# Performance work log

Hardware: AMD Instinct MI355X
Metric: run time of the kernel (lower is better)

Reference implementation:

```python
import jax, jax.numpy as jnp
import numpy as np

EPS = 1e-15  # matches torch_geometric dense pooling EPS


def gcn_conv(x, src, dst, w, W, b, n):
    # GCNConv(normalize=False): linear first, then weighted scatter-add src->dst, then bias
    h = x @ W
    msg = w[:, None] * h[src]  # [E, out]
    return jax.ops.segment_sum(msg, dst, num_segments=n) + b


def setup_inputs() -> dict:
    key = jax.random.key(0)
    ks = jax.random.split(key, 8)
    N, E, d, k = 12288, 393216, 256, 16
    x = jax.random.normal(ks[0], (N, d), dtype=jnp.float32)
    edge_index = jax.random.randint(ks[1], (2, E), 0, N, dtype=jnp.int32)
    edge_weight = jax.random.uniform(ks[2], (E,), dtype=jnp.float32)
    sc = 1.0 / np.sqrt(d).astype(np.float32)
    W1 = jax.random.normal(ks[3], (d, d), dtype=jnp.float32) * sc
    b1 = jnp.zeros((d,), jnp.float32)
    W2 = jax.random.normal(ks[4], (d, d), dtype=jnp.float32) * sc
    b2 = jnp.zeros((d,), jnp.float32)
    Wm = jax.random.normal(ks[5], (d, k), dtype=jnp.float32) * sc
    bm = jnp.zeros((k,), jnp.float32)
    return dict(x=x, edge_weight=edge_weight, W1=W1, b1=b1, W2=W2, b2=b2,
                Wm=Wm, bm=bm, edge_index=edge_index)


def reference(x, edge_weight, W1, b1, W2, b2, Wm, bm, edge_index):
    src, dst = edge_index[0], edge_index[1]
    n = x.shape[0]
    # message-passing stack: GCNConv -> ReLU -> GCNConv -> ReLU
    h = jax.nn.relu(gcn_conv(x, src, dst, edge_weight, W1, b1, n))
    h = jax.nn.relu(gcn_conv(h, src, dst, edge_weight, W2, b2, n))
    # cluster MLP (single Linear, Identity activations)
    s_logits = h @ Wm + bm  # [N, k]
    # to_dense_adj(edge_index, edge_attr=edge_weight): dense [N, N]
    adj = jnp.zeros((n, n), x.dtype).at[src, dst].add(edge_weight)
    # just_balance_pool (batch of 1)
    s = jax.nn.softmax(s_logits, axis=-1)  # [N, k]
    out = s.T @ h              # pooled features (unused by module output)
    out_adj = s.T @ adj @ s    # pooled adjacency (unused by module output)
    gram = s.T @ s             # [k, k]
    k = s.shape[-1]
    b_loss = -jnp.trace(jnp.sqrt(gram + EPS)) / jnp.sqrt(jnp.float32(n * k))
    return s, b_loss
```

## Files before the change

### kernel.cpp

```cpp
#include <hip/hip_runtime.h>
#include <hip/hip_bf16.h>
#include <hip/hip_fp16.h>

#define D 256
#define KCL 16
#define EPS 1e-15f
#define PAD 128

typedef __attribute__((ext_vector_type(8))) short short8;
typedef __attribute__((ext_vector_type(8))) _Float16 half8;
typedef __attribute__((ext_vector_type(4))) float f32x4;

__global__ __launch_bounds__(256) void setup_k(const float* __restrict__ W1,
                                               const float* __restrict__ W2,
                                               __half* __restrict__ Wt1,
                                               __half* __restrict__ Wt2,
                                               const int* __restrict__ src,
                                               const int* __restrict__ dst,
                                               const float* __restrict__ ew,
                                               int* __restrict__ deg,
                                               int2* __restrict__ edges, int E) {
    int b = blockIdx.x;
    if (b < 512) {
        const float* W = (b < 256) ? W1 : W2;
        __half* T = (b < 256) ? Wt1 : Wt2;
        int c = b & 255;
        int k = threadIdx.x;
        T[(size_t)c * D + k] = __float2half(W[(size_t)k * D + c]);
    } else {
        int e = (b - 512) * 256 + threadIdx.x;
        if (e < E) {
            int d = dst[e];
            int slot = atomicAdd(&deg[d], 1);
            if (slot < PAD)
                edges[(size_t)d * PAD + slot] = make_int2(src[e], __float_as_int(ew[e]));
        }
    }
}

__device__ __forceinline__ short8 ld8h(const float* p) {
    float4 v0 = *(const float4*)p;
    float4 v1 = *(const float4*)(p + 4);
    float vv[8] = {v0.x, v0.y, v0.z, v0.w, v1.x, v1.y, v1.z, v1.w};
    short8 o;
#pragma unroll
    for (int j = 0; j < 8; ++j) {
        _Float16 h = (_Float16)vv[j];
        o[j] = __builtin_bit_cast(short, h);
    }
    return o;
}
__device__ __forceinline__ short8 ld8h(const __half* p) {
    return *(const short8*)p;
}

template<typename T>
__global__ __launch_bounds__(256) void gemm_k(const T* __restrict__ A,
                                              const __half* __restrict__ Bt,
                                              __half* __restrict__ C) {
    __shared__ short Ah[64][40];
    int tid = threadIdx.x;
    int lane = tid & 63, w = tid >> 6;
    int bm = blockIdx.x * 64, bn = blockIdx.y * 64;
    f32x4 acc[4];
#pragma unroll
    for (int i = 0; i < 4; ++i) acc[i] = (f32x4){0.f, 0.f, 0.f, 0.f};

    int r  = tid >> 2;
    int cc = (tid & 3) * 8;
    int ar = w * 16 + (lane & 15);
    int kq = (lane >> 4) * 8;

    for (int kk = 0; kk < D; kk += 32) {
        short8 a8 = ld8h(&A[(size_t)(bm + r) * D + kk + cc]);
        __syncthreads();
        *(short8*)&Ah[r][cc] = a8;
        __syncthreads();

        half8 av = __builtin_bit_cast(half8, *(const short8*)&Ah[ar][kq]);
#pragma unroll
        for (int nf = 0; nf < 4; ++nf) {
            int col = bn + nf * 16 + (lane & 15);
            half8 bv = __builtin_bit_cast(half8,
                        *(const short8*)&Bt[(size_t)col * D + kk + kq]);
            acc[nf] = __builtin_amdgcn_mfma_f32_16x16x32_f16(av, bv, acc[nf], 0, 0, 0);
        }
    }
    int rbase = bm + w * 16 + (lane >> 4) * 4;
    int cb = bn + (lane & 15);
#pragma unroll
    for (int nf = 0; nf < 4; ++nf)
#pragma unroll
        for (int rr = 0; rr < 4; ++rr)
            C[(size_t)(rbase + rr) * D + cb + nf * 16] = __float2half(acc[nf][rr]);
}

__device__ __forceinline__ void spmm_wave(const __half* __restrict__ h,
                                          const int2* __restrict__ edges,
                                          int node, int n, int lane,
                                          int2* se, float f[4]) {
    if (lane < n) se[lane] = edges[(size_t)node * PAD + lane];
    if (lane + 64 < n) se[lane + 64] = edges[(size_t)node * PAD + lane + 64];
    float a0 = 0.f, a1 = 0.f, a2 = 0.f, a3 = 0.f;
    int i = 0;
    for (; i + 4 <= n; i += 4) {
        int2 e0 = se[i], e1 = se[i + 1], e2 = se[i + 2], e3 = se[i + 3];
        float2 r0 = ((const float2*)(h + (size_t)e0.x * D))[lane];
        float2 r1 = ((const float2*)(h + (size_t)e1.x * D))[lane];
        float2 r2 = ((const float2*)(h + (size_t)e2.x * D))[lane];
        float2 r3 = ((const float2*)(h + (size_t)e3.x * D))[lane];
        float w0 = __int_as_float(e0.y), w1 = __int_as_float(e1.y);
        float w2 = __int_as_float(e2.y), w3 = __int_as_float(e3.y);
        float2 p, q;
        p = __half22float2(__builtin_bit_cast(__half2, r0.x));
        q = __half22float2(__builtin_bit_cast(__half2, r0.y));
        a0 = fmaf(w0, p.x, a0); a1 = fmaf(w0, p.y, a1);
        a2 = fmaf(w0, q.x, a2); a3 = fmaf(w0, q.y, a3);
        p = __half22float2(__builtin_bit_cast(__half2, r1.x));
        q = __half22float2(__builtin_bit_cast(__half2, r1.y));
        a0 = fmaf(w1, p.x, a0); a1 = fmaf(w1, p.y, a1);
        a2 = fmaf(w1, q.x, a2); a3 = fmaf(w1, q.y, a3);
        p = __half22float2(__builtin_bit_cast(__half2, r2.x));
        q = __half22float2(__builtin_bit_cast(__half2, r2.y));
        a0 = fmaf(w2, p.x, a0); a1 = fmaf(w2, p.y, a1);
        a2 = fmaf(w2, q.x, a2); a3 = fmaf(w2, q.y, a3);
        p = __half22float2(__builtin_bit_cast(__half2, r3.x));
        q = __half22float2(__builtin_bit_cast(__half2, r3.y));
        a0 = fmaf(w3, p.x, a0); a1 = fmaf(w3, p.y, a1);
        a2 = fmaf(w3, q.x, a2); a3 = fmaf(w3, q.y, a3);
    }
    for (; i < n; ++i) {
        int2 e = se[i];
        float2 r = ((const float2*)(h + (size_t)e.x * D))[lane];
        float wv = __int_as_float(e.y);
        float2 p = __half22float2(__builtin_bit_cast(__half2, r.x));
        float2 q = __half22float2(__builtin_bit_cast(__half2, r.y));
        a0 = fmaf(wv, p.x, a0); a1 = fmaf(wv, p.y, a1);
        a2 = fmaf(wv, q.x, a2); a3 = fmaf(wv, q.y, a3);
    }
    f[0] = a0; f[1] = a1; f[2] = a2; f[3] = a3;
}

__global__ __launch_bounds__(256) void spmm_k(const __half* __restrict__ h,
                                              const int2* __restrict__ edges,
                                              const int* __restrict__ deg,
                                              const float* __restrict__ bias,
                                              __half* __restrict__ out) {
    __shared__ int2 se[4][PAD];
    int tid = threadIdx.x;
    int wv = tid >> 6, lane = tid & 63;
    int node = blockIdx.x * 4 + wv;
    int n = min(deg[node], PAD);
    float f[4];
    spmm_wave(h, edges, node, n, lane, se[wv], f);
    float4 bv = ((const float4*)bias)[lane];
    __half2 o01 = __float22half2_rn(make_float2(fmaxf(f[0] + bv.x, 0.f),
                                                fmaxf(f[1] + bv.y, 0.f)));
    __half2 o23 = __float22half2_rn(make_float2(fmaxf(f[2] + bv.z, 0.f),
                                                fmaxf(f[3] + bv.w, 0.f)));
    ((float2*)(out + (size_t)node * D))[lane] =
        make_float2(__builtin_bit_cast(float, o01), __builtin_bit_cast(float, o23));
}

__global__ __launch_bounds__(256) void spmm_cluster_k(const __half* __restrict__ h,
                                                      const int2* __restrict__ edges,
                                                      const int* __restrict__ deg,
                                                      const float* __restrict__ bias,
                                                      const float* __restrict__ Wm,
                                                      const float* __restrict__ bmv,
                                                      float* __restrict__ s_out) {
    __shared__ int2 se[4][PAD];
    int tid = threadIdx.x;
    int wv = tid >> 6, lane = tid & 63;
    int node = blockIdx.x * 4 + wv;
    int n = min(deg[node], PAD);
    float f[4];
    spmm_wave(h, edges, node, n, lane, se[wv], f);
    float4 bv = ((const float4*)bias)[lane];
    f[0] = fmaxf(f[0] + bv.x, 0.f); f[1] = fmaxf(f[1] + bv.y, 0.f);
    f[2] = fmaxf(f[2] + bv.z, 0.f); f[3] = fmaxf(f[3] + bv.w, 0.f);

    float pl[KCL];
#pragma unroll
    for (int j = 0; j < KCL; ++j) pl[j] = 0.f;
#pragma unroll
    for (int u = 0; u < 4; ++u) {
        const float4* wr = (const float4*)&Wm[(size_t)(4 * lane + u) * KCL];
        float fv = f[u];
#pragma unroll
        for (int q = 0; q < 4; ++q) {
            float4 a = wr[q];
            pl[q * 4 + 0] = fmaf(fv, a.x, pl[q * 4 + 0]);
            pl[q * 4 + 1] = fmaf(fv, a.y, pl[q * 4 + 1]);
            pl[q * 4 + 2] = fmaf(fv, a.z, pl[q * 4 + 2]);
            pl[q * 4 + 3] = fmaf(fv, a.w, pl[q * 4 + 3]);
        }
    }
#pragma unroll
    for (int off = 32; off; off >>= 1)
#pragma unroll
        for (int j = 0; j < KCL; ++j) pl[j] += __shfl_xor(pl[j], off, 64);
    if (lane == 0) {
        float mx = -1e30f;
#pragma unroll
        for (int j = 0; j < KCL; ++j) { pl[j] += bmv[j]; mx = fmaxf(mx, pl[j]); }
        float sum = 0.f;
#pragma unroll
        for (int j = 0; j < KCL; ++j) { pl[j] = __expf(pl[j] - mx); sum += pl[j]; }
        float inv = 1.f / sum;
        float* so = &s_out[(size_t)node * KCL];
#pragma unroll
        for (int q = 0; q < 4; ++q)
            *(float4*)&so[q * 4] = make_float4(pl[q*4+0] * inv, pl[q*4+1] * inv,
                                               pl[q*4+2] * inv, pl[q*4+3] * inv);
    }
}

__global__ __launch_bounds__(256) void sqloss_k(const float* __restrict__ s,
                                                float* __restrict__ diag,
                                                int* __restrict__ done,
                                                float* __restrict__ loss_out, int N) {
    int tid = threadIdx.x;
    int j = tid & 15;
    int g = tid >> 4;
    int total = N * KCL;
    float acc = 0.f;
    for (int idx = blockIdx.x * 256 + tid; idx < total; idx += gridDim.x * 256) {
        float v = s[idx];
        acc = fmaf(v, v, acc);
    }
    __shared__ float red[16][17];
    red[g][j] = acc;
    __syncthreads();
    if (g == 0) {
        float a = red[0][j];
#pragma unroll
        for (int gg = 1; gg < 16; ++gg) a += red[gg][j];
        atomicAdd(&diag[j], a);
    }
    __threadfence();
    __shared__ int lastFlag;
    if (tid == 0) {
        int old = atomicAdd(done, 1);
        lastFlag = (old == (int)gridDim.x - 1);
    }
    __syncthreads();
    if (lastFlag && tid == 0) {
        __threadfence();
        float sum = 0.f;
#pragma unroll
        for (int jj = 0; jj < KCL; ++jj) {
            float v = atomicAdd(&diag[jj], 0.f);
            sum += sqrtf(v + EPS);
        }
        loss_out[0] = -sum / sqrtf((float)N * (float)KCL);
    }
}

extern "C" void kernel_launch(void* const* d_in, const int* in_sizes, int n_in,
                              void* d_out, int out_size, void* d_ws, size_t ws_size,
                              hipStream_t stream) {
    const float* x  = (const float*)d_in[0];
    const float* ew = (const float*)d_in[1];
    const float* W1 = (const float*)d_in[2];
    const float* b1 = (const float*)d_in[3];
    const float* W2 = (const float*)d_in[4];
    const float* b2 = (const float*)d_in[5];
    const float* Wm = (const float*)d_in[6];
    const float* bm = (const float*)d_in[7];
    const int*   ei = (const int*)d_in[8];

    const int N = in_sizes[0] / D;
    const int E = in_sizes[1];
    const int* src = ei;
    const int* dst = ei + E;

    float* out = (float*)d_out;

    char* ws = (char*)d_ws;
    __half* G    = (__half*)ws;       ws += (size_t)N * D * 2;
    __half* H1   = (__half*)ws;       ws += (size_t)N * D * 2;
    int*   deg   = (int*)ws;          ws += (size_t)N * 4;
    float* diag  = (float*)ws;        ws += 64;
    int*   done  = (int*)ws;          ws += 16;
    int2*  edges = (int2*)ws;         ws += (size_t)N * PAD * 8;
    __half* Wt1  = (__half*)ws;       ws += (size_t)D * D * 2;
    __half* Wt2  = (__half*)ws;       ws += (size_t)D * D * 2;

    hipMemsetAsync(deg, 0, (size_t)N * 4 + 80, stream);
    int gE = (E + 255) / 256;
    setup_k<<<512 + gE, 256, 0, stream>>>(W1, W2, Wt1, Wt2,
                                          src, dst, ew, deg, edges, E);

    dim3 ggrid(N / 64, 4);
    gemm_k<float><<<ggrid, 256, 0, stream>>>(x, Wt1, G);
    spmm_k<<<N / 4, 256, 0, stream>>>(G, edges, deg, b1, H1);
    gemm_k<__half><<<ggrid, 256, 0, stream>>>(H1, Wt2, G);
    spmm_cluster_k<<<N / 4, 256, 0, stream>>>(G, edges, deg, b2, Wm, bm, out);
    sqloss_k<<<64, 256, 0, stream>>>(out, diag, done, out + (size_t)N * KCL, N);
}
```

Measured before the change: 214.0 us.

## Split SpMM feature dimension across two blocks and fuse softmax with loss

Each SpMM node is now handled by two blocks, each covering half of the 256 features, so twice as many waves are in flight for the gather-bound aggregation. Block ids are interleaved so that both halves of a node run near each other in time. The cluster projection writes per-half partial logits, and a new kernel sums them, applies softmax, and accumulates the squared-sum loss in a single pass. Edge lists are loaded with nontemporal hints. In exchange, edge lists are read twice, gather requests become 4-byte instead of 8-byte, and a partial-logit buffer is written and then read back.

```diff
diff --git a/kernel.cpp b/kernel.cpp
--- a/kernel.cpp
+++ b/kernel.cpp
@@ -6,10 +6,16 @@
 #define KCL 16
 #define EPS 1e-15f
 #define PAD 128
+#define HPF 128
 
 typedef __attribute__((ext_vector_type(8))) short short8;
 typedef __attribute__((ext_vector_type(8))) _Float16 half8;
 typedef __attribute__((ext_vector_type(4))) float f32x4;
+
+__device__ __forceinline__ int2 ntload_i2(const int2* p) {
+    long long v = __builtin_nontemporal_load((const long long*)p);
+    return *(int2*)&v;
+}
 
 __global__ __launch_bounds__(256) void setup_k(const float* __restrict__ W1,
                                                const float* __restrict__ W2,
@@ -95,149 +101,159 @@
             C[(size_t)(rbase + rr) * D + cb + nf * 16] = __float2half(acc[nf][rr]);
 }
 
-__device__ __forceinline__ void spmm_wave(const __half* __restrict__ h,
-                                          const int2* __restrict__ edges,
-                                          int node, int n, int lane,
-                                          int2* se, float f[4]) {
-    if (lane < n) se[lane] = edges[(size_t)node * PAD + lane];
-    if (lane + 64 < n) se[lane + 64] = edges[(size_t)node * PAD + lane + 64];
-    float a0 = 0.f, a1 = 0.f, a2 = 0.f, a3 = 0.f;
+__device__ __forceinline__ void spmm_wave_half(const __half* __restrict__ h,
+                                               const int2* __restrict__ edges,
+                                               int node, int half, int n, int lane,
+                                               int2* se, float& o0, float& o1) {
+    if (lane < n) se[lane] = ntload_i2(&edges[(size_t)node * PAD + lane]);
+    if (lane + 64 < n) se[lane + 64] = ntload_i2(&edges[(size_t)node * PAD + lane + 64]);
+    float a0 = 0.f, a1 = 0.f;
     int i = 0;
     for (; i + 4 <= n; i += 4) {
         int2 e0 = se[i], e1 = se[i + 1], e2 = se[i + 2], e3 = se[i + 3];
-        float2 r0 = ((const float2*)(h + (size_t)e0.x * D))[lane];
-        float2 r1 = ((const float2*)(h + (size_t)e1.x * D))[lane];
-        float2 r2 = ((const float2*)(h + (size_t)e2.x * D))[lane];
-        float2 r3 = ((const float2*)(h + (size_t)e3.x * D))[lane];
+        float r0 = ((const float*)(h + (size_t)e0.x * D + half * HPF))[lane];
+        float r1 = ((const float*)(h + (size_t)e1.x * D + half * HPF))[lane];
+        float r2 = ((const float*)(h + (size_t)e2.x * D + half * HPF))[lane];
+        float r3 = ((const float*)(h + (size_t)e3.x * D + half * HPF))[lane];
         float w0 = __int_as_float(e0.y), w1 = __int_as_float(e1.y);
         float w2 = __int_as_float(e2.y), w3 = __int_as_float(e3.y);
-        float2 p, q;
-        p = __half22float2(__builtin_bit_cast(__half2, r0.x));
-        q = __half22float2(__builtin_bit_cast(__half2, r0.y));
+        float2 p;
+        p = __half22float2(__builtin_bit_cast(__half2, r0));
         a0 = fmaf(w0, p.x, a0); a1 = fmaf(w0, p.y, a1);
-        a2 = fmaf(w0, q.x, a2); a3 = fmaf(w0, q.y, a3);
-        p = __half22float2(__builtin_bit_cast(__half2, r1.x));
-        q = __half22float2(__builtin_bit_cast(__half2, r1.y));
+        p = __half22float2(__builtin_bit_cast(__half2, r1));
         a0 = fmaf(w1, p.x, a0); a1 = fmaf(w1, p.y, a1);
-        a2 = fmaf(w1, q.x, a2); a3 = fmaf(w1, q.y, a3);
-        p = __half22float2(__builtin_bit_cast(__half2, r2.x));
-        q = __half22float2(__builtin_bit_cast(__half2, r2.y));
+        p = __half22float2(__builtin_bit_cast(__half2, r2));
         a0 = fmaf(w2, p.x, a0); a1 = fmaf(w2, p.y, a1);
-        a2 = fmaf(w2, q.x, a2); a3 = fmaf(w2, q.y, a3);
-        p = __half22float2(__builtin_bit_cast(__half2, r3.x));
-        q = __half22float2(__builtin_bit_cast(__half2, r3.y));
+        p = __half22float2(__builtin_bit_cast(__half2, r3));
         a0 = fmaf(w3, p.x, a0); a1 = fmaf(w3, p.y, a1);
-        a2 = fmaf(w3, q.x, a2); a3 = fmaf(w3, q.y, a3);
     }
     for (; i < n; ++i) {
         int2 e = se[i];
-        float2 r = ((const float2*)(h + (size_t)e.x * D))[lane];
+        float r = ((const float*)(h + (size_t)e.x * D + half * HPF))[lane];
         float wv = __int_as_float(e.y);
-        float2 p = __half22float2(__builtin_bit_cast(__half2, r.x));
-        float2 q = __half22float2(__builtin_bit_cast(__half2, r.y));
+        float2 p = __half22float2(__builtin_bit_cast(__half2, r));
         a0 = fmaf(wv, p.x, a0); a1 = fmaf(wv, p.y, a1);
-        a2 = fmaf(wv, q.x, a2); a3 = fmaf(wv, q.y, a3);
-    }
-    f[0] = a0; f[1] = a1; f[2] = a2; f[3] = a3;
-}
-
-__global__ __launch_bounds__(256) void spmm_k(const __half* __restrict__ h,
-                                              const int2* __restrict__ edges,
-                                              const int* __restrict__ deg,
-                                              const float* __restrict__ bias,
-                                              __half* __restrict__ out) {
+    }
+    o0 = a0; o1 = a1;
+}
+
+__device__ __forceinline__ void decode_bid(int bid, int& half, int& quad) {
+    half = (bid & 7) >> 2;
+    quad = ((bid >> 3) << 2) | (bid & 3);
+}
+
+__global__ __launch_bounds__(256) void spmm1_k(const __half* __restrict__ h,
+                                               const int2* __restrict__ edges,
+                                               const int* __restrict__ deg,
+                                               const float* __restrict__ bias,
+                                               __half* __restrict__ out) {
     __shared__ int2 se[4][PAD];
+    int half, quad;
+    decode_bid(blockIdx.x, half, quad);
     int tid = threadIdx.x;
     int wv = tid >> 6, lane = tid & 63;
-    int node = blockIdx.x * 4 + wv;
+    int node = quad * 4 + wv;
     int n = min(deg[node], PAD);
-    float f[4];
-    spmm_wave(h, edges, node, n, lane, se[wv], f);
-    float4 bv = ((const float4*)bias)[lane];
-    __half2 o01 = __float22half2_rn(make_float2(fmaxf(f[0] + bv.x, 0.f),
-                                                fmaxf(f[1] + bv.y, 0.f)));
-    __half2 o23 = __float22half2_rn(make_float2(fmaxf(f[2] + bv.z, 0.f),
-                                                fmaxf(f[3] + bv.w, 0.f)));
-    ((float2*)(out + (size_t)node * D))[lane] =
-        make_float2(__builtin_bit_cast(float, o01), __builtin_bit_cast(float, o23));
-}
-
-__global__ __launch_bounds__(256) void spmm_cluster_k(const __half* __restrict__ h,
-                                                      const int2* __restrict__ edges,
-                                                      const int* __restrict__ deg,
-                                                      const float* __restrict__ bias,
-                                                      const float* __restrict__ Wm,
-                                                      const float* __restrict__ bmv,
-                                                      float* __restrict__ s_out) {
+    float f0, f1;
+    spmm_wave_half(h, edges, node, half, n, lane, se[wv], f0, f1);
+    float2 bv = ((const float2*)(bias + half * HPF))[lane];
+    __half2 o = __float22half2_rn(make_float2(fmaxf(f0 + bv.x, 0.f),
+                                              fmaxf(f1 + bv.y, 0.f)));
+    __builtin_nontemporal_store(__builtin_bit_cast(unsigned, o),
+        (unsigned*)&((__half2*)(out + (size_t)node * D + half * HPF))[lane]);
+}
+
+__global__ __launch_bounds__(256) void spmm2_k(const __half* __restrict__ h,
+                                               const int2* __restrict__ edges,
+                                               const int* __restrict__ deg,
+                                               const float* __restrict__ bias,
+                                               const float* __restrict__ Wm,
+                                               float* __restrict__ part) {
     __shared__ int2 se[4][PAD];
+    int half, quad;
+    decode_bid(blockIdx.x, half, quad);
     int tid = threadIdx.x;
     int wv = tid >> 6, lane = tid & 63;
-    int node = blockIdx.x * 4 + wv;
+    int node = quad * 4 + wv;
     int n = min(deg[node], PAD);
-    float f[4];
-    spmm_wave(h, edges, node, n, lane, se[wv], f);
-    float4 bv = ((const float4*)bias)[lane];
-    f[0] = fmaxf(f[0] + bv.x, 0.f); f[1] = fmaxf(f[1] + bv.y, 0.f);
-    f[2] = fmaxf(f[2] + bv.z, 0.f); f[3] = fmaxf(f[3] + bv.w, 0.f);
-
+    float f0, f1;
+    spmm_wave_half(h, edges, node, half, n, lane, se[wv], f0, f1);
+    float2 bv = ((const float2*)(bias + half * HPF))[lane];
+    f0 = fmaxf(f0 + bv.x, 0.f);
+    f1 = fmaxf(f1 + bv.y, 0.f);
+
+    int fidx = half * HPF + 2 * lane;
     float pl[KCL];
-#pragma unroll
-    for (int j = 0; j < KCL; ++j) pl[j] = 0.f;
-#pragma unroll
-    for (int u = 0; u < 4; ++u) {
-        const float4* wr = (const float4*)&Wm[(size_t)(4 * lane + u) * KCL];
-        float fv = f[u];
-#pragma unroll
-        for (int q = 0; q < 4; ++q) {
-            float4 a = wr[q];
-            pl[q * 4 + 0] = fmaf(fv, a.x, pl[q * 4 + 0]);
-            pl[q * 4 + 1] = fmaf(fv, a.y, pl[q * 4 + 1]);
-            pl[q * 4 + 2] = fmaf(fv, a.z, pl[q * 4 + 2]);
-            pl[q * 4 + 3] = fmaf(fv, a.w, pl[q * 4 + 3]);
-        }
+    const float4* w0 = (const float4*)&Wm[(size_t)fidx * KCL];
+    const float4* w1 = (const float4*)&Wm[(size_t)(fidx + 1) * KCL];
+#pragma unroll
+    for (int q = 0; q < 4; ++q) {
+        float4 a = w0[q], b = w1[q];
+        pl[q * 4 + 0] = f0 * a.x + f1 * b.x;
+        pl[q * 4 + 1] = f0 * a.y + f1 * b.y;
+        pl[q * 4 + 2] = f0 * a.z + f1 * b.z;
+        pl[q * 4 + 3] = f0 * a.w + f1 * b.w;
     }
 #pragma unroll
     for (int off = 32; off; off >>= 1)
 #pragma unroll
         for (int j = 0; j < KCL; ++j) pl[j] += __shfl_xor(pl[j], off, 64);
     if (lane == 0) {
-        float mx = -1e30f;
-#pragma unroll
-        for (int j = 0; j < KCL; ++j) { pl[j] += bmv[j]; mx = fmaxf(mx, pl[j]); }
-        float sum = 0.f;
-#pragma unroll
-        for (int j = 0; j < KCL; ++j) { pl[j] = __expf(pl[j] - mx); sum += pl[j]; }
-        float inv = 1.f / sum;
-        float* so = &s_out[(size_t)node * KCL];
+        float* pp = &part[((size_t)node * 2 + half) * KCL];
 #pragma unroll
         for (int q = 0; q < 4; ++q)
-            *(float4*)&so[q * 4] = make_float4(pl[q*4+0] * inv, pl[q*4+1] * inv,
-                                               pl[q*4+2] * inv, pl[q*4+3] * inv);
-    }
-}
-
-__global__ __launch_bounds__(256) void sqloss_k(const float* __restrict__ s,
-                                                float* __restrict__ diag,
-                                                int* __restrict__ done,
-                                                float* __restrict__ loss_out, int N) {
+            *(float4*)&pp[q * 4] = make_float4(pl[q*4+0], pl[q*4+1],
+                                               pl[q*4+2], pl[q*4+3]);
+    }
+}
+
+__global__ __launch_bounds__(256) void softmax_loss_k(const float* __restrict__ part,
+                                                      const float* __restrict__ bmv,
+                                                      float* __restrict__ s_out,
+                                                      float* __restrict__ diag,
+                                                      int* __restrict__ done,
+                                                      float* __restrict__ loss_out,
+                                                      int N) {
     int tid = threadIdx.x;
-    int j = tid & 15;
-    int g = tid >> 4;
-    int total = N * KCL;
-    float acc = 0.f;
-    for (int idx = blockIdx.x * 256 + tid; idx < total; idx += gridDim.x * 256) {
-        float v = s[idx];
-        acc = fmaf(v, v, acc);
-    }
-    __shared__ float red[16][17];
-    red[g][j] = acc;
+    int node = blockIdx.x * 256 + tid;
+    int wv = tid >> 6, lane = tid & 63;
+    float p[KCL];
+    const float4* q0 = (const float4*)&part[(size_t)node * 2 * KCL];
+    const float4* q1 = q0 + 4;
+    const float4* bb4 = (const float4*)bmv;
+    float mx = -1e30f;
+#pragma unroll
+    for (int q = 0; q < 4; ++q) {
+        float4 a = q0[q], b = q1[q], c = bb4[q];
+        p[q*4+0] = a.x + b.x + c.x; p[q*4+1] = a.y + b.y + c.y;
+        p[q*4+2] = a.z + b.z + c.z; p[q*4+3] = a.w + b.w + c.w;
+#pragma unroll
+        for (int u = 0; u < 4; ++u) mx = fmaxf(mx, p[q*4+u]);
+    }
+    float sum = 0.f;
+#pragma unroll
+    for (int j = 0; j < KCL; ++j) { p[j] = __expf(p[j] - mx); sum += p[j]; }
+    float inv = 1.f / sum;
+    float sq[KCL];
+    float* so = &s_out[(size_t)node * KCL];
+#pragma unroll
+    for (int q = 0; q < 4; ++q) {
+        float s0 = p[q*4+0]*inv, s1 = p[q*4+1]*inv, s2 = p[q*4+2]*inv, s3 = p[q*4+3]*inv;
+        *(float4*)&so[q * 4] = make_float4(s0, s1, s2, s3);
+        sq[q*4+0] = s0*s0; sq[q*4+1] = s1*s1; sq[q*4+2] = s2*s2; sq[q*4+3] = s3*s3;
+    }
+#pragma unroll
+    for (int off = 32; off; off >>= 1)
+#pragma unroll
+        for (int j = 0; j < KCL; ++j) sq[j] += __shfl_xor(sq[j], off, 64);
+    __shared__ float red[4][KCL];
+    if (lane == 0) {
+#pragma unroll
+        for (int j = 0; j < KCL; ++j) red[wv][j] = sq[j];
+    }
     __syncthreads();
-    if (g == 0) {
-        float a = red[0][j];
-#pragma unroll
-        for (int gg = 1; gg < 16; ++gg) a += red[gg][j];
-        atomicAdd(&diag[j], a);
-    }
+    if (tid < KCL)
+        atomicAdd(&diag[tid], red[0][tid] + red[1][tid] + red[2][tid] + red[3][tid]);
     __threadfence();
     __shared__ int lastFlag;
     if (tid == 0) {
@@ -247,13 +263,13 @@
     __syncthreads();
     if (lastFlag && tid == 0) {
         __threadfence();
-        float sum = 0.f;
+        float s = 0.f;
 #pragma unroll
         for (int jj = 0; jj < KCL; ++jj) {
             float v = atomicAdd(&diag[jj], 0.f);
-            sum += sqrtf(v + EPS);
+            s += sqrtf(v + EPS);
         }
-        loss_out[0] = -sum / sqrtf((float)N * (float)KCL);
+        loss_out[0] = -s / sqrtf((float)N * (float)KCL);
     }
 }
 
@@ -286,6 +302,7 @@
     int2*  edges = (int2*)ws;         ws += (size_t)N * PAD * 8;
     __half* Wt1  = (__half*)ws;       ws += (size_t)D * D * 2;
     __half* Wt2  = (__half*)ws;       ws += (size_t)D * D * 2;
+    float* part  = (float*)ws;        ws += (size_t)N * 2 * KCL * 4;
 
     hipMemsetAsync(deg, 0, (size_t)N * 4 + 80, stream);
     int gE = (E + 255) / 256;
@@ -293,9 +310,11 @@
                                           src, dst, ew, deg, edges, E);
 
     dim3 ggrid(N / 64, 4);
+    int sgrid = (N / 4) * 2;
     gemm_k<float><<<ggrid, 256, 0, stream>>>(x, Wt1, G);
-    spmm_k<<<N / 4, 256, 0, stream>>>(G, edges, deg, b1, H1);
+    spmm1_k<<<sgrid, 256, 0, stream>>>(G, edges, deg, b1, H1);
     gemm_k<__half><<<ggrid, 256, 0, stream>>>(H1, Wt2, G);
-    spmm_cluster_k<<<N / 4, 256, 0, stream>>>(G, edges, deg, b2, Wm, bm, out);
-    sqloss_k<<<64, 256, 0, stream>>>(out, diag, done, out + (size_t)N * KCL, N);
-}
+    spmm2_k<<<sgrid, 256, 0, stream>>>(G, edges, deg, b2, Wm, part);
+    softmax_loss_k<<<48, 256, 0, stream>>>(part, bm, out, diag, done,
+                                           out + (size_t)N * KCL, N);
+}
```

After: 212.7 us. About the same (-0.6%).
